# Kernel optimization log

Hardware: AMD Instinct MI355X
Metric: run time of the kernel (lower is better)

## Reference

```python
import jax, jax.numpy as jnp
import numpy as np

EPS = 1e-6
MAX_Q = 25.0
B, M, N, S = 1024, 8192, 32, 128


def setup_inputs() -> dict:
    key = jax.random.key(0)
    k = jax.random.split(key, 6)
    z = jax.random.normal(k[0], (B, N), jnp.float32) * 1e-3
    z_j = jax.random.uniform(k[1], (M, N), jnp.float32, -1e-3, 1e-3)
    vec_d_j = jax.random.uniform(k[2], (M, N), jnp.float32, -1e-3, 1e-3)
    T_hat_j = jax.random.uniform(k[3], (M, S), jnp.float32, -1e-3, 1e-3)
    alpha_j = jnp.ones((M,), jnp.float32)
    sigma_par = jax.random.uniform(k[4], (M,), jnp.float32, 0.9, 1.5)
    sigma_perp = jax.random.uniform(k[5], (M,), jnp.float32, 0.1, 0.8)
    return {"z": z, "z_j": z_j, "vec_d_j": vec_d_j, "T_hat_j": T_hat_j,
            "alpha_j": alpha_j, "sigma_par": sigma_par, "sigma_perp": sigma_perp}


def reference(z, z_j, vec_d_j, T_hat_j, alpha_j, sigma_par, sigma_perp):
    tiny = jnp.finfo(sigma_par.dtype).eps
    w_par = 1.0 / jnp.maximum(sigma_par, tiny) ** 2      # [M]
    w_perp = 1.0 / jnp.maximum(sigma_perp, tiny) ** 2    # [M]
    w_diff = w_par - w_perp                               # [M]

    dz = z[:, None, :] - z_j[None, :, :]                  # [B, M, N]
    dz_norm_sq = jnp.sum(dz * dz, axis=-1)                # [B, M]

    d_norm = jnp.linalg.norm(vec_d_j, axis=-1, keepdims=True)  # [M, 1]
    use_proj = (d_norm > EPS).astype(z.dtype)                   # [M, 1]
    b = jnp.where(d_norm > EPS, vec_d_j / d_norm, jnp.zeros_like(vec_d_j))  # [M, N]
    proj = jnp.einsum('bmn,mn->bm', dz, b) * use_proj[:, 0][None, :]        # [B, M]

    q_pos = w_perp[None, :] * dz_norm_sq + w_diff[None, :] * (proj * proj)  # [B, M]
    q_pos = jnp.minimum(q_pos, jnp.asarray(MAX_Q, dtype=z.dtype))

    gain = alpha_j[None, :] * jnp.exp(-jnp.pi * q_pos)    # [B, M]
    T = gain @ T_hat_j                                     # [B, S]
    return T
```

## Files before the change

### kernel.cpp

```cpp
#include <hip/hip_runtime.h>
#include <hip/hip_bf16.h>
#include <math.h>

#define B_SZ 1024
#define M_SZ 8192
#define N_SZ 32
#define S_SZ 128

#define MT   256
#define BT   32
#define NTHR 256
#define NSPLIT 32

#define SG_STRIDE 264

typedef __bf16 bf16x8 __attribute__((ext_vector_type(8)));
typedef float  f32x4  __attribute__((ext_vector_type(4)));

#if defined(__has_builtin)
#if __has_builtin(__builtin_amdgcn_exp2f)
#define EXP2F(x) __builtin_amdgcn_exp2f(x)
#else
#define EXP2F(x) exp2f(x)
#endif
#else
#define EXP2F(x) exp2f(x)
#endif

#define NEG_PI_LOG2E  (-4.5323601722717285f)
#define E_CLAMP       (-113.30900573730469f)

#define WS_TSWZ   ((size_t)0)
#define WS_ZJBF   ((size_t)2 * 1024 * 1024)
#define WS_DVBF   (WS_ZJBF + (size_t)M_SZ * N_SZ * 2)
#define WS_MCONST (WS_DVBF + (size_t)M_SZ * N_SZ * 2)
#define WS_ZBF    (WS_MCONST + (size_t)M_SZ * 8 * 4)
#define WS_ZN     (WS_ZBF + (size_t)B_SZ * N_SZ * 2)
#define WS_PART   ((size_t)4 * 1024 * 1024)
#define WS_NEED   (WS_PART + (size_t)NSPLIT * B_SZ * S_SZ * 4)

__global__ __launch_bounds__(256)
void prep_kernel(const float* __restrict__ T,
                 const float* __restrict__ z,
                 const float* __restrict__ zj_in,
                 const float* __restrict__ dv_in,
                 const float* __restrict__ alpha_j,
                 const float* __restrict__ sigma_par,
                 const float* __restrict__ sigma_perp,
                 char* __restrict__ ws)
{
    const int bx = blockIdx.x;
    const int t  = threadIdx.x;

    if (bx < 512) {
        const int g    = bx * 256 + t;
        const int mc   = g >> 9;
        const int ns   = (g >> 6) & 7;
        const int lane = g & 63;
        const int c    = lane & 15;
        const int q    = lane >> 4;
        const float* src = T + (size_t)(mc * 32 + q * 8) * S_SZ + ns * 16 + c;
        bf16x8 v;
        #pragma unroll
        for (int j = 0; j < 8; ++j) v[j] = (__bf16)src[(size_t)j * S_SZ];
        *(bf16x8*)(ws + WS_TSWZ + (size_t)g * 16) = v;
    } else if (bx < 544) {
        const int m = (bx - 512) * 256 + t;
        float a[N_SZ], d[N_SZ];
        const float4* a4 = (const float4*)(zj_in + (size_t)m * N_SZ);
        const float4* d4 = (const float4*)(dv_in + (size_t)m * N_SZ);
        #pragma unroll
        for (int i = 0; i < N_SZ / 4; ++i) {
            float4 av = a4[i], dw = d4[i];
            a[4*i+0]=av.x; a[4*i+1]=av.y; a[4*i+2]=av.z; a[4*i+3]=av.w;
            d[4*i+0]=dw.x; d[4*i+1]=dw.y; d[4*i+2]=dw.z; d[4*i+3]=dw.w;
        }
        float zjn = 0.f, dnsq = 0.f, zjd = 0.f;
        #pragma unroll
        for (int n = 0; n < N_SZ; ++n) {
            zjn += a[n]*a[n]; dnsq += d[n]*d[n]; zjd += a[n]*d[n];
        }
        const float dn  = sqrtf(dnsq);
        const float inv = (dn > 1e-6f) ? (1.0f / dn) : 0.0f;
        __bf16* zjb = (__bf16*)(ws + WS_ZJBF) + (size_t)m * N_SZ;
        __bf16* dvb = (__bf16*)(ws + WS_DVBF) + (size_t)m * N_SZ;
        #pragma unroll
        for (int i = 0; i < 4; ++i) {
            bf16x8 vz, vd;
            #pragma unroll
            for (int j = 0; j < 8; ++j) {
                vz[j] = (__bf16)a[i*8+j];
                vd[j] = (__bf16)(d[i*8+j] * inv);
            }
            *(bf16x8*)(zjb + i*8) = vz;
            *(bf16x8*)(dvb + i*8) = vd;
        }
        const float tiny = 1.1920928955078125e-07f;
        const float sp  = fmaxf(sigma_par[m],  tiny);
        const float spp = fmaxf(sigma_perp[m], tiny);
        const float wperp = 1.0f / (spp * spp);
        const float wdiff = 1.0f / (sp * sp) - wperp;
        const float A = NEG_PI_LOG2E * wperp;
        float* mc8 = (float*)(ws + WS_MCONST) + (size_t)m * 8;
        *(f32x4*)mc8       = (f32x4){A, A * zjn, NEG_PI_LOG2E * wdiff, zjd * inv};
        *(f32x4*)(mc8 + 4) = (f32x4){alpha_j[m], 0.f, 0.f, 0.f};
    } else {
        const int b = (bx - 544) * 256 + t;
        float v[N_SZ];
        const float4* z4 = (const float4*)(z + (size_t)b * N_SZ);
        #pragma unroll
        for (int i = 0; i < N_SZ / 4; ++i) {
            float4 w4 = z4[i];
            v[4*i+0]=w4.x; v[4*i+1]=w4.y; v[4*i+2]=w4.z; v[4*i+3]=w4.w;
        }
        float zn = 0.f;
        #pragma unroll
        for (int n = 0; n < N_SZ; ++n) zn += v[n]*v[n];
        __bf16* zb = (__bf16*)(ws + WS_ZBF) + (size_t)b * N_SZ;
        #pragma unroll
        for (int i = 0; i < 4; ++i) {
            bf16x8 vz;
            #pragma unroll
            for (int j = 0; j < 8; ++j) vz[j] = (__bf16)v[i*8+j];
            *(bf16x8*)(zb + i*8) = vz;
        }
        ((float*)(ws + WS_ZN))[b] = zn;
    }
}

__global__ __launch_bounds__(NTHR, 4)
void cpsf_main_kernel(const char* __restrict__ ws_ro, float* __restrict__ ws_part)
{
    __shared__ __align__(16) __bf16 sG[BT * SG_STRIDE];

    const int t     = threadIdx.x;
    const int lane  = t & 63;
    const int w     = t >> 6;
    const int q     = lane >> 4;
    const int c     = lane & 15;
    const int mx    = blockIdx.x;
    const int m0    = mx * MT;
    const int bbase = blockIdx.y * BT;

    const __bf16* zbf   = (const __bf16*)(ws_ro + WS_ZBF);
    const __bf16* zjbf  = (const __bf16*)(ws_ro + WS_ZJBF);
    const __bf16* dvbf  = (const __bf16*)(ws_ro + WS_DVBF);
    const float*  mcst  = (const float*)(ws_ro + WS_MCONST);
    const float*  znp   = (const float*)(ws_ro + WS_ZN);
    const char*   Tswz  = ws_ro + WS_TSWZ;

    const int wb  = w & 1;
    const int mt0 = (w >> 1) * 8;

    const bf16x8 zA  = *(const bf16x8*)(zbf + ((size_t)(bbase + wb*16 + c) * N_SZ + q*8));
    const f32x4  zn4 = *(const f32x4*)(znp + bbase + wb*16 + q*4);

    #pragma unroll 4
    for (int ti = 0; ti < 8; ++ti) {
        const int tile = mt0 + ti;
        const int mg   = m0 + tile*16 + c;
        const bf16x8 bz = *(const bf16x8*)(zjbf + (size_t)mg * N_SZ + q*8);
        const bf16x8 bd = *(const bf16x8*)(dvbf + (size_t)mg * N_SZ + q*8);
        f32x4 s1 = __builtin_amdgcn_mfma_f32_16x16x32_bf16(zA, bz, (f32x4){0.f,0.f,0.f,0.f}, 0, 0, 0);
        f32x4 sd = __builtin_amdgcn_mfma_f32_16x16x32_bf16(zA, bd, (f32x4){0.f,0.f,0.f,0.f}, 0, 0, 0);
        const float* mc8 = mcst + (size_t)mg * 8;
        const f32x4 mc0 = *(const f32x4*)mc8;
        const float al  = mc8[4];
        #pragma unroll
        for (int reg = 0; reg < 4; ++reg) {
            const float t1 = fmaf(s1[reg], -2.0f, zn4[reg]);
            float e = fmaf(mc0[0], t1, mc0[1]);
            const float p = sd[reg] - mc0[3];
            e = fmaf(mc0[2] * p, p, e);
            e = fmaxf(e, E_CLAMP);
            const float g = al * EXP2F(e);
            sG[(size_t)(wb*16 + q*4 + reg) * SG_STRIDE + tile*16 + c] = (__bf16)g;
        }
    }
    __syncthreads();

    f32x4 acc[2][2];
    #pragma unroll
    for (int bt = 0; bt < 2; ++bt)
        #pragma unroll
        for (int i = 0; i < 2; ++i) acc[bt][i] = (f32x4){0.f,0.f,0.f,0.f};

    #pragma unroll
    for (int kc = 0; kc < MT / 32; ++kc) {
        const int mc = mx * (MT / 32) + kc;
        bf16x8 bfr[2];
        #pragma unroll
        for (int i = 0; i < 2; ++i)
            bfr[i] = *(const bf16x8*)(Tswz + ((size_t)(mc*8 + w*2 + i) * 64 + lane) * 16);
        #pragma unroll
        for (int bt = 0; bt < 2; ++bt) {
            const bf16x8 a = *(const bf16x8*)((const char*)sG
                              + (size_t)(bt*16 + c) * (SG_STRIDE*2) + kc*64 + q*16);
            #pragma unroll
            for (int i = 0; i < 2; ++i)
                acc[bt][i] = __builtin_amdgcn_mfma_f32_16x16x32_bf16(a, bfr[i], acc[bt][i], 0, 0, 0);
        }
    }

    #pragma unroll
    for (int bt = 0; bt < 2; ++bt) {
        float* part = ws_part + (size_t)mx * (B_SZ * S_SZ)
                    + (size_t)(bbase + bt*16 + q*4) * S_SZ + w*32 + c;
        #pragma unroll
        for (int i = 0; i < 2; ++i)
            #pragma unroll
            for (int reg = 0; reg < 4; ++reg)
                part[(size_t)reg * S_SZ + i*16] = acc[bt][i][reg];
    }
}

__global__ __launch_bounds__(256)
void reduce_kernel(const float* __restrict__ part, float* __restrict__ out)
{
    const int i = blockIdx.x * 256 + threadIdx.x;
    float s = 0.f;
    #pragma unroll 8
    for (int sp = 0; sp < NSPLIT; ++sp)
        s += part[(size_t)sp * (B_SZ * S_SZ) + i];
    out[i] = s;
}

#define FB_MT 256
#define FB_BT 64
#define SGF_STRIDE 68
__global__ __launch_bounds__(NTHR, 2)
void cpsf_fused_fallback(const float* __restrict__ z,
                         const float* __restrict__ z_j,
                         const float* __restrict__ vec_d_j,
                         const float* __restrict__ T_hat,
                         const float* __restrict__ alpha_j,
                         const float* __restrict__ sigma_par,
                         const float* __restrict__ sigma_perp,
                         float* __restrict__ out)
{
    __shared__ float sZ[FB_BT * N_SZ];
    __shared__ float sZn[FB_BT];
    __shared__ float sG[FB_MT * SGF_STRIDE];

    const int t     = threadIdx.x;
    const int m0    = blockIdx.x * FB_MT;
    const int bbase = blockIdx.y * FB_BT;

    {
        const float4* z4 = (const float4*)z + (size_t)bbase * (N_SZ / 4);
        float4* s4 = (float4*)sZ;
        #pragma unroll
        for (int i = t; i < FB_BT * N_SZ / 4; i += NTHR) s4[i] = z4[i];
    }
    const int m = m0 + t;
    float zj[N_SZ], dv[N_SZ];
    {
        const float4* a4 = (const float4*)(z_j     + (size_t)m * N_SZ);
        const float4* d4 = (const float4*)(vec_d_j + (size_t)m * N_SZ);
        #pragma unroll
        for (int i = 0; i < N_SZ / 4; ++i) {
            float4 av = a4[i], dw = d4[i];
            zj[4*i+0]=av.x; zj[4*i+1]=av.y; zj[4*i+2]=av.z; zj[4*i+3]=av.w;
            dv[4*i+0]=dw.x; dv[4*i+1]=dw.y; dv[4*i+2]=dw.z; dv[4*i+3]=dw.w;
        }
    }
    float zjn = 0.f, dnsq = 0.f, zjd = 0.f;
    #pragma unroll
    for (int n = 0; n < N_SZ; ++n) {
        zjn += zj[n]*zj[n]; dnsq += dv[n]*dv[n]; zjd += zj[n]*dv[n];
    }
    const float dn = sqrtf(dnsq);
    const float inv_dn = (dn > 1e-6f) ? (1.0f / dn) : 0.0f;
    const float P0 = zjd * inv_dn;
    const float tiny = 1.1920928955078125e-07f;
    const float sp  = fmaxf(sigma_par[m],  tiny);
    const float spp = fmaxf(sigma_perp[m], tiny);
    const float wperp = 1.0f / (spp * spp);
    const float wdiff = 1.0f / (sp * sp) - wperp;
    const float Cc = wperp * zjn;
    const float al = alpha_j[m];

    __syncthreads();
    if (t < FB_BT) {
        float s = 0.f;
        #pragma unroll
        for (int n = 0; n < N_SZ; ++n) { float v = sZ[t*N_SZ+n]; s += v*v; }
        sZn[t] = s;
    }
    __syncthreads();

    const float PI_F = 3.14159274101257324f;
    for (int bq = 0; bq < FB_BT / 4; ++bq) {
        float g[4];
        #pragma unroll
        for (int k = 0; k < 4; ++k) {
            const int b = bq*4 + k;
            float s1 = 0.f, sd = 0.f;
            #pragma unroll
            for (int n = 0; n < N_SZ; ++n) {
                const float zv = sZ[b*N_SZ+n];
                s1 += zv*zj[n]; sd += zv*dv[n];
            }
            const float p = sd*inv_dn - P0;
            float qv = wperp*sZn[b] - 2.0f*wperp*s1 + Cc + wdiff*p*p;
            qv = fminf(qv, 25.0f);
            g[k] = al * __expf(-PI_F*qv);
        }
        *(float4*)&sG[t*SGF_STRIDE + bq*4] = make_float4(g[0],g[1],g[2],g[3]);
    }
    __syncthreads();

    const int sg = t & 15, bg = t >> 4;
    const int b0 = bg*4, s0 = sg*8;
    float acc[4][8];
    #pragma unroll
    for (int i = 0; i < 4; ++i)
        #pragma unroll
        for (int j = 0; j < 8; ++j) acc[i][j] = 0.f;
    const float4* th4 = (const float4*)T_hat + (size_t)m0*(S_SZ/4) + sg*2;
    for (int mm = 0; mm < FB_MT; ++mm) {
        const float4 g4 = *(const float4*)&sG[mm*SGF_STRIDE + b0];
        const float4 ta = th4[(size_t)mm*(S_SZ/4)];
        const float4 tb = th4[(size_t)mm*(S_SZ/4)+1];
        const float gg[4] = {g4.x,g4.y,g4.z,g4.w};
        const float tv[8] = {ta.x,ta.y,ta.z,ta.w,tb.x,tb.y,tb.z,tb.w};
        #pragma unroll
        for (int i = 0; i < 4; ++i)
            #pragma unroll
            for (int j = 0; j < 8; ++j) acc[i][j] += gg[i]*tv[j];
    }
    float* op = out + (size_t)(bbase + b0)*S_SZ + s0;
    #pragma unroll
    for (int i = 0; i < 4; ++i)
        #pragma unroll
        for (int j = 0; j < 8; ++j)
            unsafeAtomicAdd(&op[i*S_SZ + j], acc[i][j]);
}

extern "C" void kernel_launch(void* const* d_in, const int* in_sizes, int n_in,
                              void* d_out, int out_size, void* d_ws, size_t ws_size,
                              hipStream_t stream) {
    (void)in_sizes; (void)n_in; (void)out_size;

    const float* z          = (const float*)d_in[0];
    const float* z_j        = (const float*)d_in[1];
    const float* vec_d_j    = (const float*)d_in[2];
    const float* T_hat_j    = (const float*)d_in[3];
    const float* alpha_j    = (const float*)d_in[4];
    const float* sigma_par  = (const float*)d_in[5];
    const float* sigma_perp = (const float*)d_in[6];
    float* out = (float*)d_out;

    if (ws_size >= WS_NEED) {
        char*  ws   = (char*)d_ws;
        float* part = (float*)(ws + WS_PART);

        prep_kernel<<<dim3(548), 256, 0, stream>>>(
            T_hat_j, z, z_j, vec_d_j, alpha_j, sigma_par, sigma_perp, ws);

        dim3 grid(NSPLIT, B_SZ / BT);
        cpsf_main_kernel<<<grid, NTHR, 0, stream>>>(ws, part);

        reduce_kernel<<<dim3(B_SZ * S_SZ / 256), 256, 0, stream>>>(part, out);
    } else {
        hipMemsetAsync(out, 0, (size_t)B_SZ * S_SZ * sizeof(float), stream);
        dim3 grid(M_SZ / FB_MT, B_SZ / FB_BT);
        cpsf_fused_fallback<<<grid, NTHR, 0, stream>>>(
            z, z_j, vec_d_j, T_hat_j, alpha_j, sigma_par, sigma_perp, out);
    }
}
```

Before: 96.37 us.

## Replace split-K partial buffer and reduce kernel with atomic accumulation into output

Removes the separate reduce kernel and the 16 MB partial-sum buffer. The output is zeroed by two extra blocks in the prep kernel, and each main-kernel block atomically adds its tile result into the output. NSPLIT is halved so each block loops over two 256-wide M chunks, reusing its shared-memory gain tile, which halves the number of atomic contributors. The costs are atomic contention, a nondeterministic summation order, and half as many blocks (fewer waves) in the main kernel.

```diff
diff --git a/kernel.cpp b/kernel.cpp
--- a/kernel.cpp
+++ b/kernel.cpp
@@ -7,10 +7,11 @@
 #define N_SZ 32
 #define S_SZ 128
 
-#define MT   256
-#define BT   32
-#define NTHR 256
-#define NSPLIT 32
+#define BT    32
+#define NTHR  256
+#define NSPLIT 16
+#define MT    (M_SZ / NSPLIT)
+#define MCH   256
 
 #define SG_STRIDE 264
 
@@ -36,8 +37,7 @@
 #define WS_MCONST (WS_DVBF + (size_t)M_SZ * N_SZ * 2)
 #define WS_ZBF    (WS_MCONST + (size_t)M_SZ * 8 * 4)
 #define WS_ZN     (WS_ZBF + (size_t)B_SZ * N_SZ * 2)
-#define WS_PART   ((size_t)4 * 1024 * 1024)
-#define WS_NEED   (WS_PART + (size_t)NSPLIT * B_SZ * S_SZ * 4)
+#define WS_NEED   (WS_ZN + (size_t)B_SZ * 4)
 
 __global__ __launch_bounds__(256)
 void prep_kernel(const float* __restrict__ T,
@@ -47,7 +47,8 @@
                  const float* __restrict__ alpha_j,
                  const float* __restrict__ sigma_par,
                  const float* __restrict__ sigma_perp,
-                 char* __restrict__ ws)
+                 char* __restrict__ ws,
+                 float* __restrict__ out)
 {
     const int bx = blockIdx.x;
     const int t  = threadIdx.x;
@@ -104,7 +105,7 @@
         float* mc8 = (float*)(ws + WS_MCONST) + (size_t)m * 8;
         *(f32x4*)mc8       = (f32x4){A, A * zjn, NEG_PI_LOG2E * wdiff, zjd * inv};
         *(f32x4*)(mc8 + 4) = (f32x4){alpha_j[m], 0.f, 0.f, 0.f};
-    } else {
+    } else if (bx < 548) {
         const int b = (bx - 544) * 256 + t;
         float v[N_SZ];
         const float4* z4 = (const float4*)(z + (size_t)b * N_SZ);
@@ -125,11 +126,17 @@
             *(bf16x8*)(zb + i*8) = vz;
         }
         ((float*)(ws + WS_ZN))[b] = zn;
+    } else {
+        f32x4* o4 = (f32x4*)out;
+        const int base = (bx - 548) * (B_SZ * S_SZ / 4 / 2);
+        #pragma unroll 4
+        for (int i = t; i < B_SZ * S_SZ / 4 / 2; i += 256)
+            o4[base + i] = (f32x4){0.f, 0.f, 0.f, 0.f};
     }
 }
 
 __global__ __launch_bounds__(NTHR, 4)
-void cpsf_main_kernel(const char* __restrict__ ws_ro, float* __restrict__ ws_part)
+void cpsf_main_kernel(const char* __restrict__ ws_ro, float* __restrict__ out)
 {
     __shared__ __align__(16) __bf16 sG[BT * SG_STRIDE];
 
@@ -139,7 +146,6 @@
     const int q     = lane >> 4;
     const int c     = lane & 15;
     const int mx    = blockIdx.x;
-    const int m0    = mx * MT;
     const int bbase = blockIdx.y * BT;
 
     const __bf16* zbf   = (const __bf16*)(ws_ro + WS_ZBF);
@@ -155,74 +161,68 @@
     const bf16x8 zA  = *(const bf16x8*)(zbf + ((size_t)(bbase + wb*16 + c) * N_SZ + q*8));
     const f32x4  zn4 = *(const f32x4*)(znp + bbase + wb*16 + q*4);
 
-    #pragma unroll 4
-    for (int ti = 0; ti < 8; ++ti) {
-        const int tile = mt0 + ti;
-        const int mg   = m0 + tile*16 + c;
-        const bf16x8 bz = *(const bf16x8*)(zjbf + (size_t)mg * N_SZ + q*8);
-        const bf16x8 bd = *(const bf16x8*)(dvbf + (size_t)mg * N_SZ + q*8);
-        f32x4 s1 = __builtin_amdgcn_mfma_f32_16x16x32_bf16(zA, bz, (f32x4){0.f,0.f,0.f,0.f}, 0, 0, 0);
-        f32x4 sd = __builtin_amdgcn_mfma_f32_16x16x32_bf16(zA, bd, (f32x4){0.f,0.f,0.f,0.f}, 0, 0, 0);
-        const float* mc8 = mcst + (size_t)mg * 8;
-        const f32x4 mc0 = *(const f32x4*)mc8;
-        const float al  = mc8[4];
-        #pragma unroll
-        for (int reg = 0; reg < 4; ++reg) {
-            const float t1 = fmaf(s1[reg], -2.0f, zn4[reg]);
-            float e = fmaf(mc0[0], t1, mc0[1]);
-            const float p = sd[reg] - mc0[3];
-            e = fmaf(mc0[2] * p, p, e);
-            e = fmaxf(e, E_CLAMP);
-            const float g = al * EXP2F(e);
-            sG[(size_t)(wb*16 + q*4 + reg) * SG_STRIDE + tile*16 + c] = (__bf16)g;
-        }
-    }
-    __syncthreads();
-
     f32x4 acc[2][2];
     #pragma unroll
     for (int bt = 0; bt < 2; ++bt)
         #pragma unroll
         for (int i = 0; i < 2; ++i) acc[bt][i] = (f32x4){0.f,0.f,0.f,0.f};
 
-    #pragma unroll
-    for (int kc = 0; kc < MT / 32; ++kc) {
-        const int mc = mx * (MT / 32) + kc;
-        bf16x8 bfr[2];
+    for (int chunk = 0; chunk < MT / MCH; ++chunk) {
+        const int m0 = mx * MT + chunk * MCH;
+
+        if (chunk) __syncthreads();
+
+        #pragma unroll 4
+        for (int ti = 0; ti < 8; ++ti) {
+            const int tile = mt0 + ti;
+            const int mg   = m0 + tile*16 + c;
+            const bf16x8 bz = *(const bf16x8*)(zjbf + (size_t)mg * N_SZ + q*8);
+            const bf16x8 bd = *(const bf16x8*)(dvbf + (size_t)mg * N_SZ + q*8);
+            f32x4 s1 = __builtin_amdgcn_mfma_f32_16x16x32_bf16(zA, bz, (f32x4){0.f,0.f,0.f,0.f}, 0, 0, 0);
+            f32x4 sd = __builtin_amdgcn_mfma_f32_16x16x32_bf16(zA, bd, (f32x4){0.f,0.f,0.f,0.f}, 0, 0, 0);
+            const float* mc8 = mcst + (size_t)mg * 8;
+            const f32x4 mc0 = *(const f32x4*)mc8;
+            const float al  = mc8[4];
+            #pragma unroll
+            for (int reg = 0; reg < 4; ++reg) {
+                const float t1 = fmaf(s1[reg], -2.0f, zn4[reg]);
+                float e = fmaf(mc0[0], t1, mc0[1]);
+                const float p = sd[reg] - mc0[3];
+                e = fmaf(mc0[2] * p, p, e);
+                e = fmaxf(e, E_CLAMP);
+                const float g = al * EXP2F(e);
+                sG[(size_t)(wb*16 + q*4 + reg) * SG_STRIDE + tile*16 + c] = (__bf16)g;
+            }
+        }
+        __syncthreads();
+
+        #pragma unroll
+        for (int kc = 0; kc < MCH / 32; ++kc) {
+            const int mc = (mx * MT + chunk * MCH) / 32 + kc;
+            bf16x8 bfr[2];
+            #pragma unroll
+            for (int i = 0; i < 2; ++i)
+                bfr[i] = *(const bf16x8*)(Tswz + ((size_t)(mc*8 + w*2 + i) * 64 + lane) * 16);
+            #pragma unroll
+            for (int bt = 0; bt < 2; ++bt) {
+                const bf16x8 a = *(const bf16x8*)((const char*)sG
+                                  + (size_t)(bt*16 + c) * (SG_STRIDE*2) + kc*64 + q*16);
+                #pragma unroll
+                for (int i = 0; i < 2; ++i)
+                    acc[bt][i] = __builtin_amdgcn_mfma_f32_16x16x32_bf16(a, bfr[i], acc[bt][i], 0, 0, 0);
+            }
+        }
+    }
+
+    #pragma unroll
+    for (int bt = 0; bt < 2; ++bt) {
+        float* op = out + (size_t)(bbase + bt*16 + q*4) * S_SZ + w*32 + c;
         #pragma unroll
         for (int i = 0; i < 2; ++i)
-            bfr[i] = *(const bf16x8*)(Tswz + ((size_t)(mc*8 + w*2 + i) * 64 + lane) * 16);
-        #pragma unroll
-        for (int bt = 0; bt < 2; ++bt) {
-            const bf16x8 a = *(const bf16x8*)((const char*)sG
-                              + (size_t)(bt*16 + c) * (SG_STRIDE*2) + kc*64 + q*16);
-            #pragma unroll
-            for (int i = 0; i < 2; ++i)
-                acc[bt][i] = __builtin_amdgcn_mfma_f32_16x16x32_bf16(a, bfr[i], acc[bt][i], 0, 0, 0);
-        }
-    }
-
-    #pragma unroll
-    for (int bt = 0; bt < 2; ++bt) {
-        float* part = ws_part + (size_t)mx * (B_SZ * S_SZ)
-                    + (size_t)(bbase + bt*16 + q*4) * S_SZ + w*32 + c;
-        #pragma unroll
-        for (int i = 0; i < 2; ++i)
             #pragma unroll
             for (int reg = 0; reg < 4; ++reg)
-                part[(size_t)reg * S_SZ + i*16] = acc[bt][i][reg];
-    }
-}
-
-__global__ __launch_bounds__(256)
-void reduce_kernel(const float* __restrict__ part, float* __restrict__ out)
-{
-    const int i = blockIdx.x * 256 + threadIdx.x;
-    float s = 0.f;
-    #pragma unroll 8
-    for (int sp = 0; sp < NSPLIT; ++sp)
-        s += part[(size_t)sp * (B_SZ * S_SZ) + i];
-    out[i] = s;
+                unsafeAtomicAdd(&op[(size_t)reg * S_SZ + i*16], acc[bt][i][reg]);
+    }
 }
 
 #define FB_MT 256
@@ -352,16 +352,13 @@
     float* out = (float*)d_out;
 
     if (ws_size >= WS_NEED) {
-        char*  ws   = (char*)d_ws;
-        float* part = (float*)(ws + WS_PART);
-
-        prep_kernel<<<dim3(548), 256, 0, stream>>>(
-            T_hat_j, z, z_j, vec_d_j, alpha_j, sigma_par, sigma_perp, ws);
+        char* ws = (char*)d_ws;
+
+        prep_kernel<<<dim3(550), 256, 0, stream>>>(
+            T_hat_j, z, z_j, vec_d_j, alpha_j, sigma_par, sigma_perp, ws, out);
 
         dim3 grid(NSPLIT, B_SZ / BT);
-        cpsf_main_kernel<<<grid, NTHR, 0, stream>>>(ws, part);
-
-        reduce_kernel<<<dim3(B_SZ * S_SZ / 256), 256, 0, stream>>>(part, out);
+        cpsf_main_kernel<<<grid, NTHR, 0, stream>>>(ws, out);
     } else {
         hipMemsetAsync(out, 0, (size_t)B_SZ * S_SZ * sizeof(float), stream);
         dim3 grid(M_SZ / FB_MT, B_SZ / FB_BT);
```

Result: faster. 91.93 us (-4.6%).
